# Performance work log

Measured on AMD Instinct MI355X. Metric: run time of the kernel, lower is better.

The kernel has to match this reference:

```python
import jax, jax.numpy as jnp
import numpy as np
from jax import lax

B, C, H, W = 2, 256, 48, 48
NUM_HEADS = 8
HEAD_DIM = C // NUM_HEADS
SCALE = HEAD_DIM ** (-0.5)
K1, K2 = 2, 3


def avgpool_same(y, k, pad):
    # torch AvgPool2d(kernel=k, stride=1, padding=pad), count_include_pad=True
    s = lax.reduce_window(y, 0.0, lax.add, (1, 1, k, k), (1, 1, 1, 1),
                          [(0, 0), (0, 0), (pad, pad), (pad, pad)])
    return s / (k * k)


def setup_inputs() -> dict:
    key = jax.random.key(0)
    ks = jax.random.split(key, 8)
    x = jax.random.normal(ks[0], (B, C, H, W), dtype=jnp.float32)
    y = jax.random.normal(ks[1], (B, C, H, W), dtype=jnp.float32)
    w = 0.02
    Wq = jax.random.normal(ks[2], (C, C), dtype=jnp.float32) * w
    Wkv = jax.random.normal(ks[3], (C, 2 * C), dtype=jnp.float32) * w
    Wproj = jax.random.normal(ks[4], (C, C), dtype=jnp.float32) * w
    bproj = jnp.zeros((C,), dtype=jnp.float32)
    gamma = jnp.ones((C,), dtype=jnp.float32)
    beta = jnp.zeros((C,), dtype=jnp.float32)
    attn_w1 = jnp.array([0.5], dtype=jnp.float32)
    attn_w2 = jnp.array([0.5], dtype=jnp.float32)
    return {"x": x, "y": y, "Wq": Wq, "Wkv": Wkv, "Wproj": Wproj,
            "bproj": bproj, "gamma": gamma, "beta": beta,
            "attn_w1": attn_w1, "attn_w2": attn_w2}


def _topk_branch(attn, kcount, v):
    # scatter 1.0 at top-k indices, mask everything else to -inf, softmax, @ v
    _, idx = lax.top_k(attn, kcount)                       # [B,h,N,kcount]
    mask = jnp.zeros_like(attn)
    mask = jnp.put_along_axis(mask, idx, 1.0, axis=-1, inplace=False)
    a = jnp.where(mask > 0, attn, -jnp.inf)
    a = jax.nn.softmax(a, axis=-1)
    return jnp.einsum('bhnm,bhmd->bhnd', a, v)


def reference(x, y, Wq, Wkv, Wproj, bproj, gamma, beta, attn_w1, attn_w2):
    # multi-scale avg pooling on y (all size-preserving, stride 1)
    yp = avgpool_same(y, 3, 1) + avgpool_same(y, 5, 2) + avgpool_same(y, 7, 3)
    yt = yp.reshape(B, C, H * W).transpose(0, 2, 1)        # [B, N1, C]
    mu = jnp.mean(yt, axis=-1, keepdims=True)
    var = jnp.var(yt, axis=-1, keepdims=True)
    yt = (yt - mu) / jnp.sqrt(var + 1e-5) * gamma + beta

    xt = x.reshape(B, C, H * W).transpose(0, 2, 1)         # [B, N, C]
    N = H * W
    N1 = H * W

    kv = (yt @ Wkv).reshape(B, N1, 2, NUM_HEADS, HEAD_DIM).transpose(2, 0, 3, 1, 4)
    k, v = kv[0], kv[1]                                    # [B,h,N1,hd]
    q = (xt @ Wq).reshape(B, N, NUM_HEADS, HEAD_DIM).transpose(0, 2, 1, 3)

    attn = jnp.einsum('bhnd,bhmd->bhnm', q, k) * SCALE     # [B,h,N,N1]

    out1 = _topk_branch(attn, N1 // K1, v)
    out2 = _topk_branch(attn, N1 // K2, v)
    out = out1 * attn_w1[0] + out2 * attn_w2[0]            # [B,h,N,hd]

    out = out.transpose(0, 2, 1, 3).reshape(B, N, C)
    out = out @ Wproj + bproj
    return out.transpose(0, 2, 1).reshape(B, C, H, W)
```

## Files before the change

### kernel.cpp

```cpp
#include <hip/hip_runtime.h>

#define BB     2
#define CC     256
#define HH     48
#define WW     48
#define NTOK   2304
#define NHEADS 8
#define HDIM   32
#define NBH    16
#define SCALE_QK 0.17677669529663687f
#define KSEL1  1152
#define KSEL2  768
#define NBIN   512
#define GCAP   320
#define LOSCALE 2048.0f

typedef _Float16 f16x8 __attribute__((ext_vector_type(8)));
typedef float f32x4 __attribute__((ext_vector_type(4)));

__device__ __forceinline__ int binof(float v) {
  int b = (int)((v + 1.0f) * 256.0f);
  return min(max(b, 0), NBIN - 1);
}

__global__ __launch_bounds__(256) void pool_kernel(const float* __restrict__ y,
                                                   float* __restrict__ yp) {
  __shared__ float sp[HH * WW];
  __shared__ float I[49 * 49];
  const int bc = blockIdx.x;
  const float* src = y + (size_t)bc * (HH * WW);
  for (int i = threadIdx.x; i < HH * WW; i += 256) sp[i] = src[i];
  __syncthreads();
  if (threadIdx.x < 48) {
    int r = threadIdx.x;
    float acc = 0.f;
    I[(r + 1) * 49 + 0] = 0.f;
    for (int j = 0; j < 48; ++j) { acc += sp[r * 48 + j]; I[(r + 1) * 49 + j + 1] = acc; }
  } else if (threadIdx.x < 97) {
    int j = threadIdx.x - 48;
    I[j] = 0.f;
  }
  __syncthreads();
  if (threadIdx.x < 48) {
    int j = threadIdx.x + 1;
    float acc = 0.f;
    for (int i = 1; i <= 48; ++i) { acc += I[i * 49 + j]; I[i * 49 + j] = acc; }
  }
  __syncthreads();
  for (int n = threadIdx.x; n < HH * WW; n += 256) {
    int i = n / 48, j = n % 48;
    float r = 0.f;
#pragma unroll
    for (int kk = 0; kk < 3; ++kk) {
      int p = 1 + kk;
      int i0 = i - p; if (i0 < 0) i0 = 0;
      int j0 = j - p; if (j0 < 0) j0 = 0;
      int i1 = i + p + 1; if (i1 > 48) i1 = 48;
      int j1 = j + p + 1; if (j1 > 48) j1 = 48;
      float s = I[i1 * 49 + j1] - I[i0 * 49 + j1] - I[i1 * 49 + j0] + I[i0 * 49 + j0];
      int k = 2 * p + 1;
      r += s / (float)(k * k);
    }
    yp[(size_t)bc * (HH * WW) + n] = r;
  }
}

__global__ __launch_bounds__(256) void ln_kernel(const float* __restrict__ yp,
                                                 const float* __restrict__ gamma,
                                                 const float* __restrict__ beta,
                                                 _Float16* __restrict__ yth,
                                                 _Float16* __restrict__ ytl) {
  const int bn = blockIdx.x;
  const int b = bn / NTOK, n = bn % NTOK;
  const int c = threadIdx.x;
  float v = yp[((size_t)(b * CC + c)) * NTOK + n];
  float s = v, s2 = v * v;
#pragma unroll
  for (int off = 32; off; off >>= 1) { s += __shfl_down(s, off); s2 += __shfl_down(s2, off); }
  __shared__ float ws[8];
  int wid = threadIdx.x >> 6, lane = threadIdx.x & 63;
  if (lane == 0) { ws[wid] = s; ws[4 + wid] = s2; }
  __syncthreads();
  s = ws[0] + ws[1] + ws[2] + ws[3];
  s2 = ws[4] + ws[5] + ws[6] + ws[7];
  float mean = s * (1.f / CC);
  float var = s2 * (1.f / CC) - mean * mean;
  float rstd = rsqrtf(var + 1e-5f);
  float o = (v - mean) * rstd * gamma[c] + beta[c];
  size_t dst = (size_t)bn * CC + c;
  _Float16 hi = (_Float16)o;
  yth[dst] = hi;
  ytl[dst] = (_Float16)((o - (float)hi) * LOSCALE);
}

__global__ __launch_bounds__(256) void xcast_kernel(const float* __restrict__ x,
                                                    _Float16* __restrict__ xh,
                                                    _Float16* __restrict__ xl) {
  __shared__ float tile[64][65];
  const int b = blockIdx.z;
  const int nb = blockIdx.x;
  const int cb = blockIdx.y;
  const int tid = threadIdx.x;
#pragma unroll
  for (int it = 0; it < 16; ++it) {
    int idx = it * 256 + tid;
    int cl = idx >> 6, nl = idx & 63;
    tile[cl][nl] = x[((size_t)(b * CC + cb * 64 + cl)) * NTOK + nb * 64 + nl];
  }
  __syncthreads();
#pragma unroll
  for (int it = 0; it < 16; ++it) {
    int idx = it * 256 + tid;
    int nl = idx >> 6, cl = idx & 63;
    float v = tile[cl][nl];
    size_t dst = ((size_t)(b * NTOK + nb * 64 + nl)) * CC + cb * 64 + cl;
    _Float16 hi = (_Float16)v;
    xh[dst] = hi;
    xl[dst] = (_Float16)((v - (float)hi) * LOSCALE);
  }
}

__global__ __launch_bounds__(256) void wtcast3_kernel(
    const float* __restrict__ Wq, const float* __restrict__ Wkv,
    const float* __restrict__ Wproj,
    _Float16* __restrict__ wqh, _Float16* __restrict__ wql,
    _Float16* __restrict__ wkvh, _Float16* __restrict__ wkvl,
    _Float16* __restrict__ wph, _Float16* __restrict__ wpl) {
  const int blk = blockIdx.x;
  const int k = threadIdx.x;
  const float* W; _Float16 *wh, *wl; int ncol, col; float scale;
  if (blk < CC)            { W = Wq;    wh = wqh;  wl = wql;  ncol = CC;     col = blk;          scale = SCALE_QK; }
  else if (blk < 3 * CC)   { W = Wkv;   wh = wkvh; wl = wkvl; ncol = 2 * CC; col = blk - CC;     scale = 1.0f; }
  else                     { W = Wproj; wh = wph;  wl = wpl;  ncol = CC;     col = blk - 3 * CC; scale = 1.0f; }
  float v = W[(size_t)k * ncol + col] * scale;
  _Float16 hi = (_Float16)v;
  wh[(size_t)col * CC + k] = hi;
  wl[(size_t)col * CC + k] = (_Float16)((v - (float)hi) * LOSCALE);
}

template <int MODE>
__global__ __launch_bounds__(256) void gemm_hilo_kernel(
    const _Float16* __restrict__ Ah, const _Float16* __restrict__ Al,
    const _Float16* __restrict__ Bh, const _Float16* __restrict__ Bl,
    const float* __restrict__ bias,
    _Float16* __restrict__ Oh, _Float16* __restrict__ Ol,
    _Float16* __restrict__ Ov, float* __restrict__ Of) {
  const int w = threadIdx.x >> 6;
  const int lane = threadIdx.x & 63;
  const int wm = w >> 1, wc = w & 1;
  const int r16 = lane & 15, kg = lane >> 4;
  const int m0 = blockIdx.x * 64 + wm * 32;
  const int c0 = blockIdx.y * 64 + wc * 32;
  const f32x4 fz = {0.f, 0.f, 0.f, 0.f};
  f32x4 acc00 = fz, acc01 = fz, acc10 = fz, acc11 = fz;
  f32x4 ac200 = fz, ac201 = fz, ac210 = fz, ac211 = fz;
  for (int ks = 0; ks < CC; ks += 32) {
    f16x8 ah_[2], al_[2], bh_[2], bl_[2];
#pragma unroll
    for (int i = 0; i < 2; ++i) {
      size_t offa = (size_t)(m0 + i * 16 + r16) * CC + ks + kg * 8;
      ah_[i] = *(const f16x8*)(Ah + offa);
      al_[i] = *(const f16x8*)(Al + offa);
      size_t offb = (size_t)(c0 + i * 16 + r16) * CC + ks + kg * 8;
      bh_[i] = *(const f16x8*)(Bh + offb);
      bl_[i] = *(const f16x8*)(Bl + offb);
    }
    acc00 = __builtin_amdgcn_mfma_f32_16x16x32_f16(ah_[0], bh_[0], acc00, 0, 0, 0);
    ac200 = __builtin_amdgcn_mfma_f32_16x16x32_f16(ah_[0], bl_[0], ac200, 0, 0, 0);
    ac200 = __builtin_amdgcn_mfma_f32_16x16x32_f16(al_[0], bh_[0], ac200, 0, 0, 0);
    acc01 = __builtin_amdgcn_mfma_f32_16x16x32_f16(ah_[0], bh_[1], acc01, 0, 0, 0);
    ac201 = __builtin_amdgcn_mfma_f32_16x16x32_f16(ah_[0], bl_[1], ac201, 0, 0, 0);
    ac201 = __builtin_amdgcn_mfma_f32_16x16x32_f16(al_[0], bh_[1], ac201, 0, 0, 0);
    acc10 = __builtin_amdgcn_mfma_f32_16x16x32_f16(ah_[1], bh_[0], acc10, 0, 0, 0);
    ac210 = __builtin_amdgcn_mfma_f32_16x16x32_f16(ah_[1], bl_[0], ac210, 0, 0, 0);
    ac210 = __builtin_amdgcn_mfma_f32_16x16x32_f16(al_[1], bh_[0], ac210, 0, 0, 0);
    acc11 = __builtin_amdgcn_mfma_f32_16x16x32_f16(ah_[1], bh_[1], acc11, 0, 0, 0);
    ac211 = __builtin_amdgcn_mfma_f32_16x16x32_f16(ah_[1], bl_[1], ac211, 0, 0, 0);
    ac211 = __builtin_amdgcn_mfma_f32_16x16x32_f16(al_[1], bh_[1], ac211, 0, 0, 0);
  }
  f32x4 accs[2][2] = {{acc00, acc01}, {acc10, acc11}};
  f32x4 ac2s[2][2] = {{ac200, ac201}, {ac210, ac211}};
  if constexpr (MODE == 2) {
    __shared__ float ts[4][32][33];
#pragma unroll
    for (int i = 0; i < 2; ++i)
#pragma unroll
      for (int j = 0; j < 2; ++j)
#pragma unroll
        for (int r = 0; r < 4; ++r)
          ts[w][i * 16 + kg * 4 + r][j * 16 + r16] =
              accs[i][j][r] + ac2s[i][j][r] * (1.f / LOSCALE);
    __syncthreads();
    const int b = m0 / NTOK;
    const int n_base = m0 % NTOK;
#pragma unroll
    for (int t = 0; t < 16; ++t) {
      int idx = t * 64 + lane;
      int ml = idx & 31, cl = idx >> 5;
      float v = ts[w][ml][cl] + bias[c0 + cl];
      Of[((size_t)(b * CC + c0 + cl)) * NTOK + n_base + ml] = v;
    }
  } else {
#pragma unroll
    for (int i = 0; i < 2; ++i) {
#pragma unroll
      for (int j = 0; j < 2; ++j) {
#pragma unroll
        for (int r = 0; r < 4; ++r) {
          float val = accs[i][j][r] + ac2s[i][j][r] * (1.f / LOSCALE);
          int m = m0 + i * 16 + kg * 4 + r;
          int c = c0 + j * 16 + r16;
          int b = m / NTOK, n = m % NTOK;
          if (MODE == 0 || c < CC) {
            int h = (c & (CC - 1)) >> 5, d = c & 31;
            size_t dst = ((size_t)((b * 8 + h) * NTOK) + n) * HDIM + d;
            _Float16 hi = (_Float16)val;
            Oh[dst] = hi;
            Ol[dst] = (_Float16)((val - (float)hi) * LOSCALE);
          } else {
            int cc2 = c - CC;
            int h2 = cc2 >> 5, d2 = cc2 & 31;
            Ov[((size_t)((b * NHEADS + h2) * HDIM + d2)) * NTOK + n] = (_Float16)val;
          }
        }
      }
    }
  }
}

#define SMSTEP 4
__global__ __launch_bounds__(256) void score_mfma_kernel(const _Float16* __restrict__ qh,
                                                         const _Float16* __restrict__ ql,
                                                         const _Float16* __restrict__ kh,
                                                         const _Float16* __restrict__ kl,
                                                         _Float16* __restrict__ sc, int bh0) {
  const int w = threadIdx.x >> 6;
  const int lane = threadIdx.x & 63;
  const int wn = w >> 1, wm = w & 1;
  const int r16 = lane & 15, kg = lane >> 4;
  const int z = blockIdx.z;
  const int gbh = bh0 + z;
  const size_t tb = (size_t)gbh * NTOK * HDIM;
  const int n0 = blockIdx.x * 64 + wn * 32;
  const f32x4 fz = {0.f, 0.f, 0.f, 0.f};
  f16x8 ah[2], al[2];
#pragma unroll
  for (int i = 0; i < 2; ++i) {
    size_t off = tb + (size_t)(n0 + i * 16 + r16) * HDIM + kg * 8;
    ah[i] = *(const f16x8*)(qh + off);
    al[i] = *(const f16x8*)(ql + off);
  }
  for (int s = 0; s < SMSTEP; ++s) {
    const int ms = blockIdx.y * (SMSTEP * 64) + s * 64 + wm * 32;
    f16x8 bhf[2], blf[2];
#pragma unroll
    for (int j = 0; j < 2; ++j) {
      size_t off = tb + (size_t)(ms + j * 16 + r16) * HDIM + kg * 8;
      bhf[j] = *(const f16x8*)(kh + off);
      blf[j] = *(const f16x8*)(kl + off);
    }
#pragma unroll
    for (int i = 0; i < 2; ++i)
#pragma unroll
      for (int j = 0; j < 2; ++j) {
        f32x4 acc = __builtin_amdgcn_mfma_f32_16x16x32_f16(ah[i], bhf[j], fz, 0, 0, 0);
        f32x4 ac2 = __builtin_amdgcn_mfma_f32_16x16x32_f16(ah[i], blf[j], fz, 0, 0, 0);
        ac2 = __builtin_amdgcn_mfma_f32_16x16x32_f16(al[i], bhf[j], ac2, 0, 0, 0);
        size_t rowbase = ((size_t)z * NTOK + n0 + i * 16 + kg * 4) * NTOK + ms + j * 16 + r16;
#pragma unroll
        for (int r = 0; r < 4; ++r)
          sc[rowbase + (size_t)r * NTOK] = (_Float16)(acc[r] + ac2[r] * (1.0f / LOSCALE));
      }
  }
}

template <int NPL>
__device__ __forceinline__ void radix_find(const unsigned* __restrict__ h,
                                           unsigned krem, unsigned* sres2) {
  const int lane = threadIdx.x & 63;
  unsigned c[NPL];
#pragma unroll
  for (int i = 0; i < NPL; ++i) c[i] = h[lane * NPL + i];
  unsigned suf[NPL];
  unsigned run = 0;
#pragma unroll
  for (int i = NPL - 1; i >= 0; --i) { run += c[i]; suf[i] = run; }
  unsigned acc = run;
#pragma unroll
  for (int off = 1; off < 64; off <<= 1) {
    unsigned t = __shfl_down(acc, off);
    if (lane + off < 64) acc += t;
  }
  unsigned tail = __shfl_down(acc, 1);
  if (lane == 63) tail = 0;
#pragma unroll
  for (int i = 0; i < NPL; ++i) {
    unsigned s = tail + suf[i];
    unsigned nx = (i + 1 < NPL) ? (tail + suf[i + 1]) : tail;
    if (s >= krem && nx < krem) {
      sres2[0] = (unsigned)(lane * NPL + i);
      sres2[1] = krem - nx;
    }
  }
}

__global__ __launch_bounds__(256) void select_kernel(const _Float16* __restrict__ sc,
                                                     float* __restrict__ stats,
                                                     const float* __restrict__ w1p,
                                                     const float* __restrict__ w2p) {
  __shared__ unsigned cnt[NBIN];
  __shared__ float buf[2][GCAP];
  __shared__ unsigned bcnt[2];
  __shared__ unsigned sres[4];
  __shared__ float tthr[2];
  const int tid = threadIdx.x;
  const int wv = tid >> 6, lane = tid & 63;
  const size_t base = (size_t)blockIdx.x * NTOK;
  for (int i = tid; i < NBIN; i += 256) cnt[i] = 0u;
  if (tid < 2) bcnt[tid] = 0u;
  __syncthreads();
  const bool two = (tid < (NTOK / 8 - 256));
  f16x8 r0 = *((const f16x8*)(sc + base) + tid);
  f16x8 r1 = two ? *((const f16x8*)(sc + base) + 256 + tid) : f16x8{};
#pragma unroll
  for (int e = 0; e < 8; ++e) atomicAdd(&cnt[binof((float)r0[e])], 1u);
  if (two) {
#pragma unroll
    for (int e = 0; e < 8; ++e) atomicAdd(&cnt[binof((float)r1[e])], 1u);
  }
  __syncthreads();
  if (tid < 64)       radix_find<NBIN / 64>(cnt, KSEL1, &sres[0]);
  else if (tid < 128) radix_find<NBIN / 64>(cnt, KSEL2, &sres[2]);
  __syncthreads();
  const int b1 = (int)sres[0], b2 = (int)sres[2];
  const unsigned k1 = sres[1], k2 = sres[3];
  const unsigned c1 = cnt[b1], c2 = cnt[b2];
  const bool g1ok = (c1 <= GCAP), g2ok = (c2 <= GCAP);
  const float lo1 = (b1 == 0) ? -3.4e38f : ((float)b1 * (1.f / 256.f) - 1.f);
  const float hi1 = (b1 == NBIN - 1) ? 3.4e38f : ((float)(b1 + 1) * (1.f / 256.f) - 1.f);
  const float lo2 = (b2 == 0) ? -3.4e38f : ((float)b2 * (1.f / 256.f) - 1.f);
  const float hi2 = (b2 == NBIN - 1) ? 3.4e38f : ((float)(b2 + 1) * (1.f / 256.f) - 1.f);
#pragma unroll
  for (int e = 0; e < 8; ++e) {
    float v = (float)r0[e];
    if (g1ok && v >= lo1 && v < hi1) buf[0][atomicAdd(&bcnt[0], 1u)] = v;
    if (g2ok && v >= lo2 && v < hi2) buf[1][atomicAdd(&bcnt[1], 1u)] = v;
  }
  if (two) {
#pragma unroll
    for (int e = 0; e < 8; ++e) {
      float v = (float)r1[e];
      if (g1ok && v >= lo1 && v < hi1) buf[0][atomicAdd(&bcnt[0], 1u)] = v;
      if (g2ok && v >= lo2 && v < hi2) buf[1][atomicAdd(&bcnt[1], 1u)] = v;
    }
  }
  __syncthreads();
  if (wv < 2) {
    const int sel = wv;
    const unsigned kk = sel ? k2 : k1;
    const int bb = sel ? b2 : b1;
    const unsigned cc = sel ? c2 : c1;
    if (cc <= GCAP) {
      for (unsigned i = lane; i < cc; i += 64) {
        float xv = buf[sel][i];
        unsigned g = 0, m = 0;
        for (unsigned j2 = 0; j2 < cc; ++j2) {
          float yv = buf[sel][j2];
          g += (yv > xv) ? 1u : 0u;
          m += (yv == xv) ? 1u : 0u;
        }
        if (g < kk && kk <= g + m) tthr[sel] = xv;
      }
    } else {
      for (int i = lane; i < NTOK; i += 64) {
        float xv = (float)sc[base + i];
        if (binof(xv) != bb) continue;
        unsigned g = 0, m = 0;
        for (int j2 = 0; j2 < NTOK; ++j2) {
          float yv = (float)sc[base + j2];
          if (binof(yv) != bb) continue;
          g += (yv > xv) ? 1u : 0u;
          m += (yv == xv) ? 1u : 0u;
        }
        if (g < kk && kk <= g + m) tthr[sel] = xv;
      }
    }
  }
  __syncthreads();
  if (wv < 2) {
    const int sel = wv;
    const int bb = sel ? b2 : b1;
    const unsigned cc = sel ? c2 : c1;
    const float t = tthr[sel];
    float ps = 0.f;
    if (cc <= GCAP) {
      for (unsigned i = lane; i < cc; i += 64) {
        float xv = buf[sel][i];
        if (xv >= t) ps += __expf(xv);
      }
    } else {
      for (int i = lane; i < NTOK; i += 64) {
        float xv = (float)sc[base + i];
        if (binof(xv) == bb && xv >= t) ps += __expf(xv);
      }
    }
    for (int b = bb + 1 + lane; b < NBIN; b += 64)
      ps += (float)cnt[b] * __expf((float)b * (1.f / 256.f) + (0.5f / 256.f) - 1.f);
#pragma unroll
    for (int off = 32; off; off >>= 1) ps += __shfl_down(ps, off);
    if (lane == 0) {
      float* st = stats + (size_t)blockIdx.x * 8;
      if (sel == 0) { st[0] = 0.f; st[1] = t; st[3] = w1p[0] / ps; }
      else          { st[2] = t; st[4] = w2p[0] / ps; }
    }
  }
}

__global__ __launch_bounds__(256) void ocast_kernel(const float* __restrict__ oat,
                                                    _Float16* __restrict__ oh,
                                                    _Float16* __restrict__ ol) {
  int idx = (blockIdx.x * 256 + threadIdx.x) * 4;
  f32x4 v4 = *(const f32x4*)(oat + idx);
#pragma unroll
  for (int e = 0; e < 4; ++e) {
    float v = v4[e];
    _Float16 hi = (_Float16)v;
    oh[idx + e] = hi;
    ol[idx + e] = (_Float16)((v - (float)hi) * LOSCALE);
  }
}

#define MSPLIT 4
__global__ __launch_bounds__(256) void pv_mfma_kernel(const _Float16* __restrict__ sc,
                                                      const _Float16* __restrict__ vtb,
                                                      const float* __restrict__ stats,
                                                      float* __restrict__ oat, int bh0) {
  const int w = threadIdx.x >> 6;
  const int l = threadIdx.x & 63;
  const int z = blockIdx.z;
  const int gbh = bh0 + z;
  const int b = gbh >> 3, h = gbh & 7;
  const int n0 = blockIdx.x * 64 + w * 16;
  const int row = l & 15;
  const int kg = l >> 4;
  const int n = n0 + row;
  const float* st = stats + ((size_t)z * NTOK + n) * 8;
  const float mx = st[0], t1 = st[1], t2 = st[2], w1d = st[3], w2d = st[4];
  const _Float16* srow = sc + ((size_t)z * NTOK + n) * NTOK;
  const _Float16* v0 = vtb + ((size_t)gbh * HDIM + row) * NTOK;
  const _Float16* v1 = v0 + 16 * NTOK;
  f32x4 acc0 = {0.f, 0.f, 0.f, 0.f};
  f32x4 acc1 = {0.f, 0.f, 0.f, 0.f};
  const int msteps = (NTOK / 32) / MSPLIT;
  int m0 = blockIdx.y * msteps * 32 + kg * 8;
#pragma unroll 2
  for (int s = 0; s < msteps; ++s, m0 += 32) {
    f16x8 sv8 = *(const f16x8*)(srow + m0);
    f16x8 afr;
#pragma unroll
    for (int i = 0; i < 8; ++i) {
      float sv = (float)sv8[i];
      float e = __expf(sv - mx);
      float wgt = (sv >= t1 ? w1d : 0.f) + (sv >= t2 ? w2d : 0.f);
      afr[i] = (_Float16)(e * wgt);
    }
    f16x8 bfr0 = *(const f16x8*)(v0 + m0);
    f16x8 bfr1 = *(const f16x8*)(v1 + m0);
    acc0 = __builtin_amdgcn_mfma_f32_16x16x32_f16(afr, bfr0, acc0, 0, 0, 0);
    acc1 = __builtin_amdgcn_mfma_f32_16x16x32_f16(afr, bfr1, acc1, 0, 0, 0);
  }
#pragma unroll
  for (int r = 0; r < 4; ++r) {
    int nn = n0 + kg * 4 + r;
    float* dst = &oat[((size_t)(b * NTOK + nn)) * CC + h * HDIM];
    atomicAdd(&dst[row], acc0[r]);
    atomicAdd(&dst[16 + row], acc1[r]);
  }
}

extern "C" void kernel_launch(void* const* d_in, const int* in_sizes, int n_in,
                              void* d_out, int out_size, void* d_ws, size_t ws_size,
                              hipStream_t stream) {
  const float* x     = (const float*)d_in[0];
  const float* y     = (const float*)d_in[1];
  const float* Wq    = (const float*)d_in[2];
  const float* Wkv   = (const float*)d_in[3];
  const float* Wproj = (const float*)d_in[4];
  const float* bproj = (const float*)d_in[5];
  const float* gamma = (const float*)d_in[6];
  const float* beta  = (const float*)d_in[7];
  const float* aw1   = (const float*)d_in[8];
  const float* aw2   = (const float*)d_in[9];

  float* ws = (float*)d_ws;
  const size_t SZ_PLANE = (size_t)BB * CC * NTOK;
  const size_t SZ_TBL = (size_t)NBH * NTOK * HDIM;
  float* yp    = ws;
  float* oat   = yp + SZ_PLANE;
  float* stats = oat + SZ_PLANE;
  _Float16* yth = (_Float16*)(stats + (size_t)NBH * NTOK * 8);
  _Float16* ytl = yth + SZ_PLANE;
  _Float16* xh  = ytl + SZ_PLANE;
  _Float16* xl  = xh + SZ_PLANE;
  _Float16* oh  = xl + SZ_PLANE;
  _Float16* ol  = oh + SZ_PLANE;
  _Float16* wqh = ol + SZ_PLANE;
  _Float16* wql = wqh + CC * CC;
  _Float16* wkvh = wql + CC * CC;
  _Float16* wkvl = wkvh + 2 * CC * CC;
  _Float16* wph = wkvl + 2 * CC * CC;
  _Float16* wpl = wph + CC * CC;
  _Float16* qh  = wpl + CC * CC;
  _Float16* ql  = qh + SZ_TBL;
  _Float16* kh  = ql + SZ_TBL;
  _Float16* kl  = kh + SZ_TBL;
  _Float16* vtb = kl + SZ_TBL;
  _Float16* sc  = vtb + SZ_TBL;

  const long long fixed_f = (long long)((float*)sc - ws);
  const long long avail_f = (long long)(ws_size / 4) - fixed_f;
  int CH = 8;
  while (CH > 1 && (long long)CH * NTOK * NTOK / 2 > avail_f) CH >>= 1;

  pool_kernel<<<dim3(BB * CC), 256, 0, stream>>>(y, yp);
  ln_kernel<<<dim3(BB * NTOK), 256, 0, stream>>>(yp, gamma, beta, yth, ytl);
  xcast_kernel<<<dim3(NTOK / 64, CC / 64, BB), 256, 0, stream>>>(x, xh, xl);
  wtcast3_kernel<<<dim3(4 * CC), 256, 0, stream>>>(Wq, Wkv, Wproj, wqh, wql,
                                                   wkvh, wkvl, wph, wpl);
  gemm_hilo_kernel<0><<<dim3(BB * NTOK / 64, CC / 64), 256, 0, stream>>>(
      xh, xl, wqh, wql, nullptr, qh, ql, nullptr, nullptr);
  gemm_hilo_kernel<1><<<dim3(BB * NTOK / 64, 2 * CC / 64), 256, 0, stream>>>(
      yth, ytl, wkvh, wkvl, nullptr, kh, kl, vtb, nullptr);

  hipMemsetAsync(oat, 0, SZ_PLANE * sizeof(float), stream);

  const int nch = NBH / CH;
  for (int ch = 0; ch < nch; ++ch) {
    int bh0 = ch * CH;
    score_mfma_kernel<<<dim3(NTOK / 64, NTOK / (SMSTEP * 64), CH), 256, 0, stream>>>(
        qh, ql, kh, kl, sc, bh0);
    select_kernel<<<dim3(CH * NTOK), 256, 0, stream>>>(sc, stats, aw1, aw2);
    pv_mfma_kernel<<<dim3(NTOK / 64, MSPLIT, CH), 256, 0, stream>>>(sc, vtb, stats, oat, bh0);
  }

  ocast_kernel<<<dim3(SZ_PLANE / 1024), 256, 0, stream>>>(oat, oh, ol);
  gemm_hilo_kernel<2><<<dim3(BB * NTOK / 64, CC / 64), 256, 0, stream>>>(
      oh, ol, wph, wpl, bproj, nullptr, nullptr, nullptr, (float*)d_out);
}
```

Measured before the change: 340.1 us.

## Tile layernorm, fuse output hi/lo split into proj GEMM, parallelize select tail

Three changes. The layernorm kernel now handles a tile of 32 tokens per block, staging through shared memory, so reads are coalesced and fp16 writes are vectorized. The separate ocast kernel is removed: the projection GEMM reads fp32 attention output directly and splits it into hi/lo halves in registers. The select kernel's threshold search and exp-sum now use all four waves instead of two, combining partial sums through shared memory. Together these aim to cut launch count, memory traffic and serialized work, at the cost of repeated conversion work inside the GEMM.

```diff
diff --git a/kernel.cpp b/kernel.cpp
--- a/kernel.cpp
+++ b/kernel.cpp
@@ -70,27 +70,49 @@
                                                  const float* __restrict__ beta,
                                                  _Float16* __restrict__ yth,
                                                  _Float16* __restrict__ ytl) {
-  const int bn = blockIdx.x;
-  const int b = bn / NTOK, n = bn % NTOK;
-  const int c = threadIdx.x;
-  float v = yp[((size_t)(b * CC + c)) * NTOK + n];
-  float s = v, s2 = v * v;
-#pragma unroll
-  for (int off = 32; off; off >>= 1) { s += __shfl_down(s, off); s2 += __shfl_down(s2, off); }
-  __shared__ float ws[8];
-  int wid = threadIdx.x >> 6, lane = threadIdx.x & 63;
-  if (lane == 0) { ws[wid] = s; ws[4 + wid] = s2; }
-  __syncthreads();
-  s = ws[0] + ws[1] + ws[2] + ws[3];
-  s2 = ws[4] + ws[5] + ws[6] + ws[7];
-  float mean = s * (1.f / CC);
-  float var = s2 * (1.f / CC) - mean * mean;
-  float rstd = rsqrtf(var + 1e-5f);
-  float o = (v - mean) * rstd * gamma[c] + beta[c];
-  size_t dst = (size_t)bn * CC + c;
-  _Float16 hi = (_Float16)o;
-  yth[dst] = hi;
-  ytl[dst] = (_Float16)((o - (float)hi) * LOSCALE);
+  __shared__ float tile[CC][33];
+  __shared__ float part[8][32];
+  __shared__ float part2[8][32];
+  const int b = blockIdx.y;
+  const int n0 = blockIdx.x * 32;
+  const int tid = threadIdx.x;
+#pragma unroll
+  for (int it = 0; it < 32; ++it) {
+    int idx = it * 256 + tid;
+    int c = idx >> 5, nl = idx & 31;
+    tile[c][nl] = yp[((size_t)(b * CC + c)) * NTOK + n0 + nl];
+  }
+  __syncthreads();
+  const int nl = tid & 31, cs = tid >> 5;
+  float s = 0.f, s2 = 0.f;
+#pragma unroll
+  for (int i = 0; i < 32; ++i) {
+    float v = tile[cs * 32 + i][nl];
+    s += v; s2 += v * v;
+  }
+  part[cs][nl] = s; part2[cs][nl] = s2;
+  __syncthreads();
+  float S = 0.f, S2 = 0.f;
+#pragma unroll
+  for (int i = 0; i < 8; ++i) { S += part[i][nl]; S2 += part2[i][nl]; }
+  const float mean = S * (1.f / CC);
+  const float var = S2 * (1.f / CC) - mean * mean;
+  const float rstd = rsqrtf(var + 1e-5f);
+  const size_t dstb = ((size_t)(b * NTOK + n0 + nl)) * CC + cs * 32;
+#pragma unroll
+  for (int g8 = 0; g8 < 4; ++g8) {
+    f16x8 vh, vl;
+#pragma unroll
+    for (int e = 0; e < 8; ++e) {
+      int c = cs * 32 + g8 * 8 + e;
+      float o = (tile[c][nl] - mean) * rstd * gamma[c] + beta[c];
+      _Float16 hi = (_Float16)o;
+      vh[e] = hi;
+      vl[e] = (_Float16)((o - (float)hi) * LOSCALE);
+    }
+    *(f16x8*)(yth + dstb + g8 * 8) = vh;
+    *(f16x8*)(ytl + dstb + g8 * 8) = vl;
+  }
 }
 
 __global__ __launch_bounds__(256) void xcast_kernel(const float* __restrict__ x,
@@ -141,6 +163,7 @@
 template <int MODE>
 __global__ __launch_bounds__(256) void gemm_hilo_kernel(
     const _Float16* __restrict__ Ah, const _Float16* __restrict__ Al,
+    const float* __restrict__ Af,
     const _Float16* __restrict__ Bh, const _Float16* __restrict__ Bl,
     const float* __restrict__ bias,
     _Float16* __restrict__ Oh, _Float16* __restrict__ Ol,
@@ -159,8 +182,22 @@
 #pragma unroll
     for (int i = 0; i < 2; ++i) {
       size_t offa = (size_t)(m0 + i * 16 + r16) * CC + ks + kg * 8;
-      ah_[i] = *(const f16x8*)(Ah + offa);
-      al_[i] = *(const f16x8*)(Al + offa);
+      if constexpr (MODE == 2) {
+        f32x4 a0 = *(const f32x4*)(Af + offa);
+        f32x4 a1 = *(const f32x4*)(Af + offa + 4);
+#pragma unroll
+        for (int e = 0; e < 4; ++e) {
+          _Float16 h0 = (_Float16)a0[e];
+          ah_[i][e] = h0;
+          al_[i][e] = (_Float16)((a0[e] - (float)h0) * LOSCALE);
+          _Float16 h1 = (_Float16)a1[e];
+          ah_[i][e + 4] = h1;
+          al_[i][e + 4] = (_Float16)((a1[e] - (float)h1) * LOSCALE);
+        }
+      } else {
+        ah_[i] = *(const f16x8*)(Ah + offa);
+        al_[i] = *(const f16x8*)(Al + offa);
+      }
       size_t offb = (size_t)(c0 + i * 16 + r16) * CC + ks + kg * 8;
       bh_[i] = *(const f16x8*)(Bh + offb);
       bl_[i] = *(const f16x8*)(Bl + offb);
@@ -313,6 +350,7 @@
   __shared__ unsigned bcnt[2];
   __shared__ unsigned sres[4];
   __shared__ float tthr[2];
+  __shared__ float psw[4];
   const int tid = threadIdx.x;
   const int wv = tid >> 6, lane = tid & 63;
   const size_t base = (size_t)blockIdx.x * NTOK;
@@ -355,13 +393,13 @@
     }
   }
   __syncthreads();
-  if (wv < 2) {
-    const int sel = wv;
+  {
+    const int sel = wv & 1, half = wv >> 1;
     const unsigned kk = sel ? k2 : k1;
     const int bb = sel ? b2 : b1;
     const unsigned cc = sel ? c2 : c1;
     if (cc <= GCAP) {
-      for (unsigned i = lane; i < cc; i += 64) {
+      for (unsigned i = half * 64 + lane; i < cc; i += 128) {
         float xv = buf[sel][i];
         unsigned g = 0, m = 0;
         for (unsigned j2 = 0; j2 < cc; ++j2) {
@@ -371,7 +409,7 @@
         }
         if (g < kk && kk <= g + m) tthr[sel] = xv;
       }
-    } else {
+    } else if (half == 0) {
       for (int i = lane; i < NTOK; i += 64) {
         float xv = (float)sc[base + i];
         if (binof(xv) != bb) continue;
@@ -387,46 +425,39 @@
     }
   }
   __syncthreads();
-  if (wv < 2) {
-    const int sel = wv;
+  {
+    const int sel = wv & 1, half = wv >> 1;
     const int bb = sel ? b2 : b1;
     const unsigned cc = sel ? c2 : c1;
     const float t = tthr[sel];
     float ps = 0.f;
     if (cc <= GCAP) {
-      for (unsigned i = lane; i < cc; i += 64) {
+      for (unsigned i = half * 64 + lane; i < cc; i += 128) {
         float xv = buf[sel][i];
         if (xv >= t) ps += __expf(xv);
       }
-    } else {
+    } else if (half == 0) {
       for (int i = lane; i < NTOK; i += 64) {
         float xv = (float)sc[base + i];
         if (binof(xv) == bb && xv >= t) ps += __expf(xv);
       }
     }
-    for (int b = bb + 1 + lane; b < NBIN; b += 64)
+    for (int b = bb + 1 + half * 64 + lane; b < NBIN; b += 128)
       ps += (float)cnt[b] * __expf((float)b * (1.f / 256.f) + (0.5f / 256.f) - 1.f);
 #pragma unroll
     for (int off = 32; off; off >>= 1) ps += __shfl_down(ps, off);
-    if (lane == 0) {
-      float* st = stats + (size_t)blockIdx.x * 8;
-      if (sel == 0) { st[0] = 0.f; st[1] = t; st[3] = w1p[0] / ps; }
-      else          { st[2] = t; st[4] = w2p[0] / ps; }
-    }
-  }
-}
-
-__global__ __launch_bounds__(256) void ocast_kernel(const float* __restrict__ oat,
-                                                    _Float16* __restrict__ oh,
-                                                    _Float16* __restrict__ ol) {
-  int idx = (blockIdx.x * 256 + threadIdx.x) * 4;
-  f32x4 v4 = *(const f32x4*)(oat + idx);
-#pragma unroll
-  for (int e = 0; e < 4; ++e) {
-    float v = v4[e];
-    _Float16 hi = (_Float16)v;
-    oh[idx + e] = hi;
-    ol[idx + e] = (_Float16)((v - (float)hi) * LOSCALE);
+    if (lane == 0) psw[wv] = ps;
+  }
+  __syncthreads();
+  if (tid == 0) {
+    float D1 = psw[0] + psw[2];
+    float D2 = psw[1] + psw[3];
+    float* st = stats + (size_t)blockIdx.x * 8;
+    st[0] = 0.f;
+    st[1] = tthr[0];
+    st[2] = tthr[1];
+    st[3] = w1p[0] / D1;
+    st[4] = w2p[0] / D2;
   }
 }
 
@@ -502,9 +533,7 @@
   _Float16* ytl = yth + SZ_PLANE;
   _Float16* xh  = ytl + SZ_PLANE;
   _Float16* xl  = xh + SZ_PLANE;
-  _Float16* oh  = xl + SZ_PLANE;
-  _Float16* ol  = oh + SZ_PLANE;
-  _Float16* wqh = ol + SZ_PLANE;
+  _Float16* wqh = xl + SZ_PLANE;
   _Float16* wql = wqh + CC * CC;
   _Float16* wkvh = wql + CC * CC;
   _Float16* wkvl = wkvh + 2 * CC * CC;
@@ -523,14 +552,14 @@
   while (CH > 1 && (long long)CH * NTOK * NTOK / 2 > avail_f) CH >>= 1;
 
   pool_kernel<<<dim3(BB * CC), 256, 0, stream>>>(y, yp);
-  ln_kernel<<<dim3(BB * NTOK), 256, 0, stream>>>(yp, gamma, beta, yth, ytl);
+  ln_kernel<<<dim3(NTOK / 32, BB), 256, 0, stream>>>(yp, gamma, beta, yth, ytl);
   xcast_kernel<<<dim3(NTOK / 64, CC / 64, BB), 256, 0, stream>>>(x, xh, xl);
   wtcast3_kernel<<<dim3(4 * CC), 256, 0, stream>>>(Wq, Wkv, Wproj, wqh, wql,
                                                    wkvh, wkvl, wph, wpl);
   gemm_hilo_kernel<0><<<dim3(BB * NTOK / 64, CC / 64), 256, 0, stream>>>(
-      xh, xl, wqh, wql, nullptr, qh, ql, nullptr, nullptr);
+      xh, xl, nullptr, wqh, wql, nullptr, qh, ql, nullptr, nullptr);
   gemm_hilo_kernel<1><<<dim3(BB * NTOK / 64, 2 * CC / 64), 256, 0, stream>>>(
-      yth, ytl, wkvh, wkvl, nullptr, kh, kl, vtb, nullptr);
+      yth, ytl, nullptr, wkvh, wkvl, nullptr, kh, kl, vtb, nullptr);
 
   hipMemsetAsync(oat, 0, SZ_PLANE * sizeof(float), stream);
 
@@ -543,7 +572,6 @@
     pv_mfma_kernel<<<dim3(NTOK / 64, MSPLIT, CH), 256, 0, stream>>>(sc, vtb, stats, oat, bh0);
   }
 
-  ocast_kernel<<<dim3(SZ_PLANE / 1024), 256, 0, stream>>>(oat, oh, ol);
   gemm_hilo_kernel<2><<<dim3(BB * NTOK / 64, CC / 64), 256, 0, stream>>>(
-      oh, ol, wph, wpl, bproj, nullptr, nullptr, nullptr, (float*)d_out);
-}
+      nullptr, nullptr, oat, wph, wpl, bproj, nullptr, nullptr, nullptr, (float*)d_out);
+}
```

Measured after the change: 336.6 us. No clear change (-1.0%).
